# Optimization experiments

Measured on AMD Instinct MI355X. Metric: run time of the kernel, lower is better.

## Reference

```python
import jax, jax.numpy as jnp
import numpy as np

WS = (2, 7, 7)   # window size (d, h, w)
NH = 4           # num heads
EPS = 1e-5       # LayerNorm eps (torch default)


def _rel_index():
    wd, wh, ww = WS
    coords = np.stack(np.meshgrid(np.arange(wd), np.arange(wh), np.arange(ww), indexing='ij'))  # (3,wd,wh,ww)
    cf = coords.reshape(3, -1)                      # (3, N)
    rel = cf[:, :, None] - cf[:, None, :]           # (3, N, N)
    rel = rel.transpose(1, 2, 0).astype(np.int64)   # (N, N, 3)
    rel[..., 0] += wd - 1
    rel[..., 1] += wh - 1
    rel[..., 2] += ww - 1
    rel[..., 0] *= (2 * wh - 1) * (2 * ww - 1)
    rel[..., 1] *= (2 * ww - 1)
    return jnp.asarray(rel.sum(-1), dtype=jnp.int32)  # (N, N)


def setup_inputs() -> dict:
    key = jax.random.key(0)
    ks = jax.random.split(key, 6)
    C, CH = 128, 512
    TBL = (2 * WS[0] - 1) * (2 * WS[1] - 1) * (2 * WS[2] - 1)  # 507
    rn = lambda k, s, sc=0.02: jax.random.normal(k, s, jnp.float32) * sc
    return {
        'x': jax.random.normal(ks[0], (2, 8, 56, 56, C), jnp.float32),
        'norm1_w': jnp.ones((C,), jnp.float32), 'norm1_b': jnp.zeros((C,), jnp.float32),
        'qkv_w': rn(ks[1], (3 * C, C)), 'qkv_b': jnp.zeros((3 * C,), jnp.float32),
        'bias_table': rn(ks[2], (TBL, NH)),
        'proj_w': rn(ks[3], (C, C)), 'proj_b': jnp.zeros((C,), jnp.float32),
        'norm2_w': jnp.ones((C,), jnp.float32), 'norm2_b': jnp.zeros((C,), jnp.float32),
        'fc1_w': rn(ks[4], (CH, C)), 'fc1_b': jnp.zeros((CH,), jnp.float32),
        'fc2_w': rn(ks[5], (C, CH)), 'fc2_b': jnp.zeros((C,), jnp.float32),
        'rel_index': _rel_index(),
    }


def _layernorm(x, w, b):
    m = jnp.mean(x, axis=-1, keepdims=True)
    v = jnp.mean(jnp.square(x - m), axis=-1, keepdims=True)
    return (x - m) * jax.lax.rsqrt(v + EPS) * w + b


def reference(x, norm1_w, norm1_b, qkv_w, qkv_b, bias_table, proj_w, proj_b,
              norm2_w, norm2_b, fc1_w, fc1_b, fc2_w, fc2_b, rel_index):
    B, D, H, W, C = x.shape
    wd, wh, ww = WS
    N = wd * wh * ww
    hd = C // NH

    shortcut = x
    xn = _layernorm(x, norm1_w, norm1_b)
    # window partition: (B,D,H,W,C) -> (B*nW, N, C)
    xw = xn.reshape(B, D // wd, wd, H // wh, wh, W // ww, ww, C)
    xw = xw.transpose(0, 1, 3, 5, 2, 4, 6, 7).reshape(-1, N, C)
    B_ = xw.shape[0]

    qkv = (xw @ qkv_w.T + qkv_b).reshape(B_, N, 3, NH, hd).transpose(2, 0, 3, 1, 4)
    q, k, v = qkv[0] * (hd ** -0.5), qkv[1], qkv[2]   # (B_, NH, N, hd)
    attn = jnp.einsum('bhnd,bhmd->bhnm', q, k)
    bias = bias_table[rel_index.reshape(-1)].reshape(N, N, NH).transpose(2, 0, 1)  # (NH,N,N)
    attn = jax.nn.softmax(attn + bias[None], axis=-1)
    out = jnp.einsum('bhnm,bhmd->bhnd', attn, v).transpose(0, 2, 1, 3).reshape(B_, N, C)
    out = out @ proj_w.T + proj_b

    # window reverse: (B*nW, N, C) -> (B,D,H,W,C)
    xr = out.reshape(B, D // wd, H // wh, W // ww, wd, wh, ww, C)
    xr = xr.transpose(0, 1, 4, 2, 5, 3, 6, 7).reshape(B, D, H, W, C)

    x = shortcut + xr
    h = _layernorm(x, norm2_w, norm2_b)
    h = jax.nn.gelu(h @ fc1_w.T + fc1_b, approximate=False)  # torch nn.GELU = exact erf
    return x + (h @ fc2_w.T + fc2_b)
```

## Files before the change

kernel.cpp:

```cpp
#include <hip/hip_runtime.h>
#include <hip/hip_bf16.h>

typedef __hip_bfloat16 bf16;
typedef unsigned short u16t;
typedef unsigned int u32t;
typedef __attribute__((ext_vector_type(8))) short bf16x8_t;
typedef __attribute__((ext_vector_type(4))) float f32x4_t;

#define DEVI static __device__ __forceinline__

DEVI float u2f(u32t bits) { union { u32t u; float f; } v; v.u = bits; return v.f; }
DEVI float bflo(u32t u) { return u2f((u & 0xffffu) << 16); }
DEVI float bfhi(u32t u) { return u2f(u & 0xffff0000u); }
DEVI float sh2f(short s) { return u2f(((u32t)(u16t)s) << 16); }
DEVI float bf2f(bf16 h) { return __bfloat162float(h); }
DEVI bf16 f2bf(float f) { return __float2bfloat16(f); }
DEVI u16t f2bfbits(float f) {
  bf16 h = __float2bfloat16(f);
  union { bf16 h; u16t u; } v; v.h = h; return v.u;
}

DEVI void gl_lds16(const void* g, void* l) {
  __builtin_amdgcn_global_load_lds(
      (const __attribute__((address_space(1))) unsigned int*)g,
      (__attribute__((address_space(3))) unsigned int*)l, 16, 0, 0);
}

#define TOK   50176
#define NWIN  512
#define NTOK  98
#define NHEAD 4
#define HDIM  32
#define QSCALE 0.17677669529663687f

__global__ __launch_bounds__(256) void setup_k(
    const float* __restrict__ a, const float* __restrict__ b,
    const float* __restrict__ c, const float* __restrict__ d,
    bf16* __restrict__ o,
    const float* __restrict__ btab, const int* __restrict__ relidx,
    const float* __restrict__ qkv_b, float* __restrict__ BmatT,
    float* __restrict__ bsc) {
  int bx = blockIdx.x;
  if (bx < 768) {
    int i = bx * 256 + threadIdx.x;
    const float* s; int off;
    if (i < 49152)       { s = a; off = 0; }
    else if (i < 65536)  { s = b; off = 49152; }
    else if (i < 131072) { s = c; off = 65536; }
    else                 { s = d; off = 131072; }
    float v = s[i - off];
    if (i < 16384) v *= QSCALE;
    o[i] = f2bf(v);
  } else {
    int idx = (bx - 768) * 256 + threadIdx.x;
    if (idx < NTOK * NTOK) {
      int i = idx / NTOK, j = idx - i * NTOK;
      int r = relidx[idx] * NHEAD;
#pragma unroll
      for (int h = 0; h < NHEAD; h++)
        BmatT[(size_t)(h * NTOK + j) * 112 + i] = btab[r + h];
    }
    if (bx == 768 && threadIdx.x < 384)
      bsc[threadIdx.x] = qkv_b[threadIdx.x] * (threadIdx.x < 128 ? QSCALE : 1.0f);
  }
}

DEVI int winrev(int grow) {
  int nw = grow / NTOK, n = grow - nw * NTOK;
  int wq = nw & 7, hq = (nw >> 3) & 7, dq = (nw >> 6) & 3, bb = nw >> 8;
  int wr = n % 7; int q7 = n / 7; int hr = q7 % 7, dr = q7 / 7;
  return ((bb * 8 + dq * 2 + dr) * 56 + hq * 7 + hr) * 56 + wq * 7 + wr;
}

__global__ __launch_bounds__(256) void qkvln_k(
    const float* __restrict__ x, const float* __restrict__ n1w,
    const float* __restrict__ n1b, const bf16* __restrict__ W,
    const float* __restrict__ bsc, bf16* __restrict__ qkvO)
{
  __shared__ __align__(16) short As[64 * 128];
  __shared__ __align__(16) short Bs[128 * 128];
  const int tid = threadIdx.x;
  const int rowBase = blockIdx.x << 6;
  const int wv = tid >> 6, lane = tid & 63;
  const int q = lane >> 4, r16 = lane & 15;

#pragma unroll
  for (int t = 0; t < 8; t++) {
    int f = tid + (t << 8);
    int row = f >> 4, cs = (f & 15) ^ (row & 15);
    gl_lds16((const u16t*)W + (size_t)row * 128 + (cs << 3), &Bs[f << 3]);
  }

  {
    const int c = lane << 1;
    float lw0 = n1w[c], lw1 = n1w[c + 1];
    float lb0 = n1b[c], lb1 = n1b[c + 1];
#pragma unroll
    for (int rr = 0; rr < 16; rr++) {
      int row = (wv << 4) + rr;
      int tt = winrev(rowBase + row);
      float2 xv = *(const float2*)(x + (size_t)tt * 128 + c);
      float x0 = xv.x, x1 = xv.y;
      float s = x0 + x1, ss = x0 * x0 + x1 * x1;
#pragma unroll
      for (int m = 32; m; m >>= 1) { s += __shfl_xor(s, m); ss += __shfl_xor(ss, m); }
      float mean = s * 0.0078125f;
      float var = ss * 0.0078125f - mean * mean;
      float rstd = rsqrtf(var + 1e-5f);
      float y0 = (x0 - mean) * rstd * lw0 + lb0;
      float y1 = (x1 - mean) * rstd * lw1 + lb1;
      u32t ov = ((u32t)f2bfbits(y1) << 16) | (u32t)f2bfbits(y0);
      int slot = (lane >> 2) ^ (row & 15);
      *(u32t*)&As[(row << 7) + (slot << 3) + ((lane & 3) << 1)] = ov;
    }
  }
  __syncthreads();

#pragma unroll 1
  for (int qt = 0; qt < 3; qt++) {
    if (qt > 0) {
#pragma unroll
      for (int t = 0; t < 8; t++) {
        int f = tid + (t << 8);
        int row = f >> 4, cs = (f & 15) ^ (row & 15);
        gl_lds16((const u16t*)W + (size_t)((qt << 7) + row) * 128 + (cs << 3),
                 &Bs[f << 3]);
      }
      __syncthreads();
    }
    f32x4_t acc[8];
#pragma unroll
    for (int j = 0; j < 8; j++) acc[j] = (f32x4_t){0.f, 0.f, 0.f, 0.f};
#pragma unroll
    for (int ks = 0; ks < 4; ks++) {
      int rowA = (wv << 4) + r16;
      int slotA = ((ks << 2) + q) ^ (rowA & 15);
      bf16x8_t af = *(const bf16x8_t*)&As[(rowA << 7) + (slotA << 3)];
      bf16x8_t bfr[8];
#pragma unroll
      for (int nt = 0; nt < 8; nt++) {
        int row = (nt << 4) + r16;
        int slot = ((ks << 2) + q) ^ (row & 15);
        bfr[nt] = *(const bf16x8_t*)&Bs[(row << 7) + (slot << 3)];
      }
#pragma unroll
      for (int nt = 0; nt < 8; nt++)
        acc[nt] = __builtin_amdgcn_mfma_f32_16x16x32_bf16(af, bfr[nt], acc[nt], 0, 0, 0);
    }
    float bv[8];
#pragma unroll
    for (int nt = 0; nt < 8; nt++) bv[nt] = bsc[(qt << 7) + (nt << 4) + r16];
    __syncthreads();
#pragma unroll
    for (int reg = 0; reg < 4; reg++) {
      int lrow = (wv << 4) + (q << 2) + reg;
#pragma unroll
      for (int nt = 0; nt < 8; nt++)
        Bs[(lrow << 7) + (nt << 4) + r16] = (short)f2bfbits(acc[nt][reg] + bv[nt]);
    }
    __syncthreads();
#pragma unroll
    for (int t = 0; t < 4; t++) {
      int f = tid + (t << 8);
      int row = f >> 4, c8 = (f & 15) << 3;
      size_t ob = (size_t)(rowBase + row) * 384 + (qt << 7) + c8;
      *(uint4*)((u16t*)qkvO + ob) = *(const uint4*)&Bs[(row << 7) + c8];
    }
    if (qt < 2) __syncthreads();
  }
}

__global__ __launch_bounds__(512, 4) void proj_k(
    const bf16* __restrict__ A, const bf16* __restrict__ W,
    const float* __restrict__ bias, const float* __restrict__ resX,
    bf16* __restrict__ outB, bf16* __restrict__ outB2,
    const float* __restrict__ lnw, const float* __restrict__ lnb)
{
  __shared__ __align__(16) short As[128 * 128];
  __shared__ __align__(16) short Bs[128 * 128];
  const int tid = threadIdx.x;
  const int rowBase = blockIdx.x << 7;
  const int wv = tid >> 6, lane = tid & 63;
  const int q = lane >> 4, r16 = lane & 15;
  const int mB = wv << 4;

#pragma unroll
  for (int t = 0; t < 4; t++) {
    int f = tid + (t << 9);
    int row = f >> 4, cs = (f & 15) ^ (row & 15);
    gl_lds16((const u16t*)A + (size_t)(rowBase + row) * 128 + (cs << 3),
             &As[f << 3]);
  }
#pragma unroll
  for (int t = 0; t < 4; t++) {
    int f = tid + (t << 9);
    int row = f >> 4, cs = (f & 15) ^ (row & 15);
    gl_lds16((const u16t*)W + (size_t)row * 128 + (cs << 3), &Bs[f << 3]);
  }
  __syncthreads();

  f32x4_t acc[8];
#pragma unroll
  for (int j = 0; j < 8; j++) acc[j] = (f32x4_t){0.f, 0.f, 0.f, 0.f};
#pragma unroll
  for (int ks = 0; ks < 4; ks++) {
    int rowA = mB + r16;
    int slotA = ((ks << 2) + q) ^ (rowA & 15);
    bf16x8_t af = *(const bf16x8_t*)&As[(rowA << 7) + (slotA << 3)];
    bf16x8_t bfr[8];
#pragma unroll
    for (int nt = 0; nt < 8; nt++) {
      int row = (nt << 4) + r16;
      int slot = ((ks << 2) + q) ^ (row & 15);
      bfr[nt] = *(const bf16x8_t*)&Bs[(row << 7) + (slot << 3)];
    }
#pragma unroll
    for (int nt = 0; nt < 8; nt++)
      acc[nt] = __builtin_amdgcn_mfma_f32_16x16x32_bf16(af, bfr[nt], acc[nt], 0, 0, 0);
  }
  __syncthreads();

  float bv[8];
#pragma unroll
  for (int nt = 0; nt < 8; nt++) bv[nt] = bias[(nt << 4) + r16];

#pragma unroll
  for (int reg = 0; reg < 4; reg++) {
    int lrow = mB + (q << 2) + reg;
#pragma unroll
    for (int nt = 0; nt < 8; nt++)
      As[(lrow << 7) + (nt << 4) + r16] = (short)f2bfbits(acc[nt][reg] + bv[nt]);
  }
  __syncthreads();
#pragma unroll
  for (int t = 0; t < 4; t++) {
    int f = tid + (t << 9);
    int row = f >> 4, c8 = (f & 15) << 3;
    int tt = winrev(rowBase + row);
    size_t ob = (size_t)tt * 128 + c8;
    float4 r0 = *(const float4*)(resX + ob);
    float4 r1 = *(const float4*)(resX + ob + 4);
    short* cs = &As[(row << 7) + c8];
    u16t pk[8];
    pk[0] = f2bfbits(sh2f(cs[0]) + r0.x); pk[1] = f2bfbits(sh2f(cs[1]) + r0.y);
    pk[2] = f2bfbits(sh2f(cs[2]) + r0.z); pk[3] = f2bfbits(sh2f(cs[3]) + r0.w);
    pk[4] = f2bfbits(sh2f(cs[4]) + r1.x); pk[5] = f2bfbits(sh2f(cs[5]) + r1.y);
    pk[6] = f2bfbits(sh2f(cs[6]) + r1.z); pk[7] = f2bfbits(sh2f(cs[7]) + r1.w);
    *(uint4*)((u16t*)outB + ob) = *(const uint4*)pk;
    *(uint4*)cs = *(const uint4*)pk;
  }
  __syncthreads();
  const int c = lane << 1;
  float2 lw = *(const float2*)(lnw + c);
  float2 lb = *(const float2*)(lnb + c);
#pragma unroll 4
  for (int rr = 0; rr < 16; rr++) {
    int row = (wv << 4) + rr;
    u32t u = *(const u32t*)&As[(row << 7) + c];
    float x0 = bflo(u), x1 = bfhi(u);
    float s = x0 + x1, ss = x0 * x0 + x1 * x1;
#pragma unroll
    for (int m = 32; m; m >>= 1) { s += __shfl_xor(s, m); ss += __shfl_xor(ss, m); }
    float mean = s * 0.0078125f;
    float var = ss * 0.0078125f - mean * mean;
    float rstd = rsqrtf(var + 1e-5f);
    float y0 = (x0 - mean) * rstd * lw.x + lb.x;
    float y1 = (x1 - mean) * rstd * lw.y + lb.y;
    int tt = winrev(rowBase + row);
    u32t ov = ((u32t)f2bfbits(y1) << 16) | (u32t)f2bfbits(y0);
    *(u32t*)((u16t*)outB2 + (size_t)tt * 128 + c) = ov;
  }
}

__global__ __launch_bounds__(512, 4) void mlp_fused_k(
    const bf16* __restrict__ Axn, const bf16* __restrict__ F1,
    const bf16* __restrict__ F2, const float* __restrict__ b1,
    const float* __restrict__ b2, const bf16* __restrict__ resB,
    float* __restrict__ out)
{
  __shared__ __align__(16) char smem[81920];
  short* As  = (short*)smem;
  short* F1s = (short*)(smem + 32768);
  short* F2s = (short*)(smem + 49152);
  short* Hs  = (short*)(smem + 65536);
  float* Cf  = (float*)smem;

  const int tid = threadIdx.x;
  const int rowBase = blockIdx.x << 7;
  const int wv = tid >> 6, lane = tid & 63;
  const int q = lane >> 4, r16 = lane & 15;
  const int mB = wv << 4;

#pragma unroll
  for (int t = 0; t < 4; t++) {
    int f = tid + (t << 9);
    int row = f >> 4, cs = (f & 15) ^ (row & 15);
    gl_lds16((const u16t*)Axn + (size_t)(rowBase + row) * 128 + (cs << 3),
             &As[f << 3]);
  }
#pragma unroll
  for (int t = 0; t < 2; t++) {
    int f = tid + (t << 9);
    int row = f >> 4, cs = (f & 15) ^ (row & 15);
    gl_lds16((const u16t*)F1 + (size_t)row * 128 + (cs << 3), &F1s[f << 3]);
  }
#pragma unroll
  for (int t = 0; t < 2; t++) {
    int f = tid + (t << 9);
    int row = f >> 3, cs = (f & 7) ^ (row & 7);
    gl_lds16((const u16t*)F2 + (size_t)row * 512 + (cs << 3), &F2s[f << 3]);
  }
  __syncthreads();

  f32x4_t oacc[8];
#pragma unroll
  for (int j = 0; j < 8; j++) oacc[j] = (f32x4_t){0.f, 0.f, 0.f, 0.f};

#pragma unroll 1
  for (int c = 0; c < 8; c++) {
    if (c > 0) {
#pragma unroll
      for (int t = 0; t < 2; t++) {
        int f = tid + (t << 9);
        int row = f >> 4, cs = (f & 15) ^ (row & 15);
        gl_lds16((const u16t*)F1 + (size_t)(c * 64 + row) * 128 + (cs << 3),
                 &F1s[f << 3]);
      }
#pragma unroll
      for (int t = 0; t < 2; t++) {
        int f = tid + (t << 9);
        int row = f >> 3, cs = (f & 7) ^ (row & 7);
        gl_lds16((const u16t*)F2 + (size_t)row * 512 + c * 64 + (cs << 3),
                 &F2s[f << 3]);
      }
      __syncthreads();
    }

    f32x4_t hacc[4];
#pragma unroll
    for (int j = 0; j < 4; j++) hacc[j] = (f32x4_t){0.f, 0.f, 0.f, 0.f};
#pragma unroll
    for (int ks = 0; ks < 4; ks++) {
      int rowA = mB + r16;
      int slotA = ((ks << 2) + q) ^ (rowA & 15);
      bf16x8_t af = *(const bf16x8_t*)&As[(rowA << 7) + (slotA << 3)];
      bf16x8_t bfr[4];
#pragma unroll
      for (int nt = 0; nt < 4; nt++) {
        int row = (nt << 4) + r16;
        int slot = ((ks << 2) + q) ^ (row & 15);
        bfr[nt] = *(const bf16x8_t*)&F1s[(row << 7) + (slot << 3)];
      }
#pragma unroll
      for (int nt = 0; nt < 4; nt++)
        hacc[nt] = __builtin_amdgcn_mfma_f32_16x16x32_bf16(af, bfr[nt], hacc[nt], 0, 0, 0);
    }

    float bb[4];
#pragma unroll
    for (int nt = 0; nt < 4; nt++) bb[nt] = b1[c * 64 + (nt << 4) + r16];
#pragma unroll
    for (int reg = 0; reg < 4; reg++) {
      int lrow = mB + (q << 2) + reg;
#pragma unroll
      for (int nt = 0; nt < 4; nt++) {
        float v = hacc[nt][reg] + bb[nt];
        v = 0.5f * v * (1.0f + erff(v * 0.70710678118654752f));
        int col = (nt << 4) + r16;
        int sp = (col >> 3) ^ (lrow & 7);
        Hs[(lrow << 6) + (sp << 3) + (col & 7)] = (short)f2bfbits(v);
      }
    }
    __syncthreads();

#pragma unroll
    for (int ks = 0; ks < 2; ks++) {
      int rowA = mB + r16;
      int slotA = ((ks << 2) + q) ^ (rowA & 7);
      bf16x8_t af = *(const bf16x8_t*)&Hs[(rowA << 6) + (slotA << 3)];
      bf16x8_t bfr[8];
#pragma unroll
      for (int nt = 0; nt < 8; nt++) {
        int row = (nt << 4) + r16;
        int slot = ((ks << 2) + q) ^ (row & 7);
        bfr[nt] = *(const bf16x8_t*)&F2s[(row << 6) + (slot << 3)];
      }
#pragma unroll
      for (int nt = 0; nt < 8; nt++)
        oacc[nt] = __builtin_amdgcn_mfma_f32_16x16x32_bf16(af, bfr[nt], oacc[nt], 0, 0, 0);
    }
    __syncthreads();
  }

  float bv[8];
#pragma unroll
  for (int nt = 0; nt < 8; nt++) bv[nt] = b2[(nt << 4) + r16];
#pragma unroll
  for (int reg = 0; reg < 4; reg++) {
    int lrow = mB + (q << 2) + reg;
#pragma unroll
    for (int nt = 0; nt < 8; nt++)
      Cf[lrow * 132 + (nt << 4) + r16] = oacc[nt][reg] + bv[nt];
  }
  __syncthreads();
#pragma unroll
  for (int t = 0; t < 8; t++) {
    int f = tid + (t << 9);
    int row = f >> 5, c4 = (f & 31) << 2;
    size_t ob = (size_t)(rowBase + row) * 128 + c4;
    const u16t* rp = (const u16t*)resB + ob;
    const float* cp = &Cf[row * 132 + c4];
    float4 v;
    v.x = cp[0] + sh2f(rp[0]);
    v.y = cp[1] + sh2f(rp[1]);
    v.z = cp[2] + sh2f(rp[2]);
    v.w = cp[3] + sh2f(rp[3]);
    *(float4*)(out + ob) = v;
  }
}

#define PSTR 136
__global__ __launch_bounds__(256) void attn_mfma_k(
    const bf16* __restrict__ qkv, const float* __restrict__ BmatT,
    bf16* __restrict__ out)
{
  __shared__ short Vt[32 * PSTR];
  __shared__ short Ps[112 * PSTR];
  const int nw = blockIdx.x, h = blockIdx.y;
  const int tid = threadIdx.x;
  const int wv = tid >> 6, lane = tid & 63;
  const int q = lane >> 4, r16 = lane & 15;

  for (int idx = tid; idx < 32 * 38; idx += 256) {
    int d = idx / 38, j = 98 + idx % 38;
    Vt[d * PSTR + j] = 0;
  }
  for (int idx = tid; idx < 112 * 12; idx += 256) {
    int r = idx / 12, c = (idx % 12) << 1;
    *(u32t*)&Ps[r * PSTR + 112 + c] = 0;
  }
  for (int idx = tid; idx < NTOK * 16; idx += 256) {
    int j = idx >> 4, d2 = (idx & 15) << 1;
    u32t uv = *(const u32t*)((const u16t*)qkv +
                             (size_t)(nw * NTOK + j) * 384 + 256 + h * 32 + d2);
    Vt[d2 * PSTR + j] = (short)(uv & 0xffffu);
    Vt[(d2 + 1) * PSTR + j] = (short)(uv >> 16);
  }
  __syncthreads();

  const int mt0 = wv;
  const bool has2 = (wv + 4) < 7;
  const int mt1 = has2 ? wv + 4 : wv;

  int i0 = mt0 * 16 + r16; if (i0 > NTOK - 1) i0 = NTOK - 1;
  int i1 = mt1 * 16 + r16; if (i1 > NTOK - 1) i1 = NTOK - 1;
  bf16x8_t aq0 = *(const bf16x8_t*)((const u16t*)qkv +
      (size_t)(nw * NTOK + i0) * 384 + h * 32 + (q << 3));
  bf16x8_t aq1 = *(const bf16x8_t*)((const u16t*)qkv +
      (size_t)(nw * NTOK + i1) * 384 + h * 32 + (q << 3));

  f32x4_t sc[2][7];
#pragma unroll
  for (int nt = 0; nt < 7; nt++) {
    int j = (nt << 4) + r16; if (j > NTOK - 1) j = NTOK - 1;
    const float* bRow = &BmatT[(size_t)(h * NTOK + j) * 112];
    bf16x8_t bk = *(const bf16x8_t*)((const u16t*)qkv +
        (size_t)(nw * NTOK + j) * 384 + 128 + h * 32 + (q << 3));
    f32x4_t b0 = *(const f32x4_t*)&bRow[mt0 * 16 + (q << 2)];
    f32x4_t b1 = *(const f32x4_t*)&bRow[mt1 * 16 + (q << 2)];
    sc[0][nt] = __builtin_amdgcn_mfma_f32_16x16x32_bf16(aq0, bk, b0, 0, 0, 0);
    sc[1][nt] = __builtin_amdgcn_mfma_f32_16x16x32_bf16(aq1, bk, b1, 0, 0, 0);
  }

#pragma unroll
  for (int sel = 0; sel < 2; sel++) {
    if (sel == 1 && !has2) break;
    int mtile = sel ? mt1 : mt0;
    int ibase = mtile * 16 + (q << 2);
    float s[4][7];
#pragma unroll
    for (int nt = 0; nt < 7; nt++) {
      int j = (nt << 4) + r16;
#pragma unroll
      for (int reg = 0; reg < 4; reg++) {
        int i = ibase + reg;
        s[reg][nt] = (i < NTOK && j < NTOK) ? sc[sel][nt][reg] : -1.0e30f;
      }
    }
#pragma unroll
    for (int reg = 0; reg < 4; reg++) {
      float m = -3.0e38f;
#pragma unroll
      for (int nt = 0; nt < 7; nt++) m = fmaxf(m, s[reg][nt]);
#pragma unroll
      for (int d = 8; d; d >>= 1) m = fmaxf(m, __shfl_xor(m, d));
      float sum = 0.f;
#pragma unroll
      for (int nt = 0; nt < 7; nt++) { s[reg][nt] = __expf(s[reg][nt] - m); sum += s[reg][nt]; }
#pragma unroll
      for (int d = 8; d; d >>= 1) sum += __shfl_xor(sum, d);
      float inv = 1.f / sum;
#pragma unroll
      for (int nt = 0; nt < 7; nt++)
        Ps[(ibase + reg) * PSTR + (nt << 4) + r16] =
            (short)f2bfbits(s[reg][nt] * inv);
    }
    f32x4_t o0 = {0.f, 0.f, 0.f, 0.f}, o1 = {0.f, 0.f, 0.f, 0.f};
#pragma unroll
    for (int kt = 0; kt < 4; kt++) {
      bf16x8_t ap = *(const bf16x8_t*)&Ps[(mtile * 16 + r16) * PSTR + (kt << 5) + (q << 3)];
      bf16x8_t bv0 = *(const bf16x8_t*)&Vt[r16 * PSTR + (kt << 5) + (q << 3)];
      bf16x8_t bv1 = *(const bf16x8_t*)&Vt[(16 + r16) * PSTR + (kt << 5) + (q << 3)];
      o0 = __builtin_amdgcn_mfma_f32_16x16x32_bf16(ap, bv0, o0, 0, 0, 0);
      o1 = __builtin_amdgcn_mfma_f32_16x16x32_bf16(ap, bv1, o1, 0, 0, 0);
    }
#pragma unroll
    for (int reg = 0; reg < 4; reg++) {
      int i = mtile * 16 + (q << 2) + reg;
      if (i < NTOK) {
        size_t ob = (size_t)(nw * NTOK + i) * 128 + h * 32;
        out[ob + r16] = f2bf(o0[reg]);
        out[ob + 16 + r16] = f2bf(o1[reg]);
      }
    }
  }
}

extern "C" void kernel_launch(void* const* d_in, const int* in_sizes, int n_in,
                              void* d_out, int out_size, void* d_ws, size_t ws_size,
                              hipStream_t stream) {
  const float* x      = (const float*)d_in[0];
  const float* n1w    = (const float*)d_in[1];
  const float* n1b    = (const float*)d_in[2];
  const float* qkv_w  = (const float*)d_in[3];
  const float* qkv_b  = (const float*)d_in[4];
  const float* btab   = (const float*)d_in[5];
  const float* proj_w = (const float*)d_in[6];
  const float* proj_b = (const float*)d_in[7];
  const float* n2w    = (const float*)d_in[8];
  const float* n2b    = (const float*)d_in[9];
  const float* fc1_w  = (const float*)d_in[10];
  const float* fc1_b  = (const float*)d_in[11];
  const float* fc2_w  = (const float*)d_in[12];
  const float* fc2_b  = (const float*)d_in[13];
  const int*   relidx = (const int*)d_in[14];

  const size_t Asz = (size_t)TOK * 128 * 2;
  char* ws = (char*)d_ws;
  bf16* wbf   = (bf16*)ws;
  bf16* qkvw16  = wbf;
  bf16* projw16 = wbf + 49152;
  bf16* fc1w16  = wbf + 65536;
  bf16* fc2w16  = wbf + 131072;
  float* BmatT = (float*)(ws + 393216);
  float* bsc   = (float*)(ws + 393216 + 175616);
  char* R = ws + (1 << 20);
  bf16* attn  = (bf16*)d_out;
  bf16* qkv   = (bf16*)R;
  bf16* x2    = (bf16*)R;
  bf16* xn2   = (bf16*)(R + Asz);
  float* out  = (float*)d_out;

  setup_k<<<806, 256, 0, stream>>>(qkv_w, proj_w, fc1_w, fc2_w, wbf,
                                   btab, relidx, qkv_b, BmatT, bsc);
  qkvln_k<<<TOK / 64, 256, 0, stream>>>(x, n1w, n1b, qkvw16, bsc, qkv);
  attn_mfma_k<<<dim3(NWIN, NHEAD), 256, 0, stream>>>(qkv, BmatT, attn);
  proj_k<<<TOK / 128, 512, 0, stream>>>(
      attn, projw16, proj_b, x, x2, xn2, n2w, n2b);
  mlp_fused_k<<<TOK / 128, 512, 0, stream>>>(
      xn2, fc1w16, fc2w16, fc1_b, fc2_b, x2, out);
}
```

Before: 207.3 us.

## Fuse projection, residual, LayerNorm2 and MLP into one kernel

Merges the projection kernel and the fused MLP kernel into a single kernel. The projected+residual tile and its LayerNorm result now stay in LDS, and the residual x2 is kept in registers, so the intermediate x2/xn2 bf16 buffers are no longer written to and re-read from global memory, and one launch is removed. The MLP output is now scattered back to window-reversed token positions in the final buffer. The cost is higher register pressure from the 16 held residual words. There is also a possible cross-block hazard: the attention input also lives in the output buffer, so one block's output writes could overwrite attention rows another block has not yet read.

```diff
diff --git a/kernel.cpp b/kernel.cpp
--- a/kernel.cpp
+++ b/kernel.cpp
@@ -170,14 +170,22 @@
   }
 }
 
-__global__ __launch_bounds__(512, 4) void proj_k(
-    const bf16* __restrict__ A, const bf16* __restrict__ W,
-    const float* __restrict__ bias, const float* __restrict__ resX,
-    bf16* __restrict__ outB, bf16* __restrict__ outB2,
-    const float* __restrict__ lnw, const float* __restrict__ lnb)
+__global__ __launch_bounds__(512, 4) void projmlp_k(
+    const bf16* __restrict__ A, const bf16* __restrict__ Wp,
+    const float* __restrict__ pb, const float* __restrict__ resX,
+    const float* __restrict__ lnw, const float* __restrict__ lnb,
+    const bf16* __restrict__ F1, const bf16* __restrict__ F2,
+    const float* __restrict__ b1, const float* __restrict__ b2,
+    float* __restrict__ out)
 {
-  __shared__ __align__(16) short As[128 * 128];
-  __shared__ __align__(16) short Bs[128 * 128];
+  __shared__ __align__(16) char smem[81920];
+  short* As  = (short*)smem;
+  short* Bs  = (short*)(smem + 32768);
+  short* F1s = (short*)(smem + 32768);
+  short* F2s = (short*)(smem + 49152);
+  short* Hs  = (short*)(smem + 65536);
+  float* Cf  = (float*)smem;
+
   const int tid = threadIdx.x;
   const int rowBase = blockIdx.x << 7;
   const int wv = tid >> 6, lane = tid & 63;
@@ -195,7 +203,7 @@
   for (int t = 0; t < 4; t++) {
     int f = tid + (t << 9);
     int row = f >> 4, cs = (f & 15) ^ (row & 15);
-    gl_lds16((const u16t*)W + (size_t)row * 128 + (cs << 3), &Bs[f << 3]);
+    gl_lds16((const u16t*)Wp + (size_t)row * 128 + (cs << 3), &Bs[f << 3]);
   }
   __syncthreads();
 
@@ -220,84 +228,6 @@
   }
   __syncthreads();
 
-  float bv[8];
-#pragma unroll
-  for (int nt = 0; nt < 8; nt++) bv[nt] = bias[(nt << 4) + r16];
-
-#pragma unroll
-  for (int reg = 0; reg < 4; reg++) {
-    int lrow = mB + (q << 2) + reg;
-#pragma unroll
-    for (int nt = 0; nt < 8; nt++)
-      As[(lrow << 7) + (nt << 4) + r16] = (short)f2bfbits(acc[nt][reg] + bv[nt]);
-  }
-  __syncthreads();
-#pragma unroll
-  for (int t = 0; t < 4; t++) {
-    int f = tid + (t << 9);
-    int row = f >> 4, c8 = (f & 15) << 3;
-    int tt = winrev(rowBase + row);
-    size_t ob = (size_t)tt * 128 + c8;
-    float4 r0 = *(const float4*)(resX + ob);
-    float4 r1 = *(const float4*)(resX + ob + 4);
-    short* cs = &As[(row << 7) + c8];
-    u16t pk[8];
-    pk[0] = f2bfbits(sh2f(cs[0]) + r0.x); pk[1] = f2bfbits(sh2f(cs[1]) + r0.y);
-    pk[2] = f2bfbits(sh2f(cs[2]) + r0.z); pk[3] = f2bfbits(sh2f(cs[3]) + r0.w);
-    pk[4] = f2bfbits(sh2f(cs[4]) + r1.x); pk[5] = f2bfbits(sh2f(cs[5]) + r1.y);
-    pk[6] = f2bfbits(sh2f(cs[6]) + r1.z); pk[7] = f2bfbits(sh2f(cs[7]) + r1.w);
-    *(uint4*)((u16t*)outB + ob) = *(const uint4*)pk;
-    *(uint4*)cs = *(const uint4*)pk;
-  }
-  __syncthreads();
-  const int c = lane << 1;
-  float2 lw = *(const float2*)(lnw + c);
-  float2 lb = *(const float2*)(lnb + c);
-#pragma unroll 4
-  for (int rr = 0; rr < 16; rr++) {
-    int row = (wv << 4) + rr;
-    u32t u = *(const u32t*)&As[(row << 7) + c];
-    float x0 = bflo(u), x1 = bfhi(u);
-    float s = x0 + x1, ss = x0 * x0 + x1 * x1;
-#pragma unroll
-    for (int m = 32; m; m >>= 1) { s += __shfl_xor(s, m); ss += __shfl_xor(ss, m); }
-    float mean = s * 0.0078125f;
-    float var = ss * 0.0078125f - mean * mean;
-    float rstd = rsqrtf(var + 1e-5f);
-    float y0 = (x0 - mean) * rstd * lw.x + lb.x;
-    float y1 = (x1 - mean) * rstd * lw.y + lb.y;
-    int tt = winrev(rowBase + row);
-    u32t ov = ((u32t)f2bfbits(y1) << 16) | (u32t)f2bfbits(y0);
-    *(u32t*)((u16t*)outB2 + (size_t)tt * 128 + c) = ov;
-  }
-}
-
-__global__ __launch_bounds__(512, 4) void mlp_fused_k(
-    const bf16* __restrict__ Axn, const bf16* __restrict__ F1,
-    const bf16* __restrict__ F2, const float* __restrict__ b1,
-    const float* __restrict__ b2, const bf16* __restrict__ resB,
-    float* __restrict__ out)
-{
-  __shared__ __align__(16) char smem[81920];
-  short* As  = (short*)smem;
-  short* F1s = (short*)(smem + 32768);
-  short* F2s = (short*)(smem + 49152);
-  short* Hs  = (short*)(smem + 65536);
-  float* Cf  = (float*)smem;
-
-  const int tid = threadIdx.x;
-  const int rowBase = blockIdx.x << 7;
-  const int wv = tid >> 6, lane = tid & 63;
-  const int q = lane >> 4, r16 = lane & 15;
-  const int mB = wv << 4;
-
-#pragma unroll
-  for (int t = 0; t < 4; t++) {
-    int f = tid + (t << 9);
-    int row = f >> 4, cs = (f & 15) ^ (row & 15);
-    gl_lds16((const u16t*)Axn + (size_t)(rowBase + row) * 128 + (cs << 3),
-             &As[f << 3]);
-  }
 #pragma unroll
   for (int t = 0; t < 2; t++) {
     int f = tid + (t << 9);
@@ -309,6 +239,63 @@
     int f = tid + (t << 9);
     int row = f >> 3, cs = (f & 7) ^ (row & 7);
     gl_lds16((const u16t*)F2 + (size_t)row * 512 + (cs << 3), &F2s[f << 3]);
+  }
+
+  float pbv[8];
+#pragma unroll
+  for (int nt = 0; nt < 8; nt++) pbv[nt] = pb[(nt << 4) + r16];
+#pragma unroll
+  for (int reg = 0; reg < 4; reg++) {
+    int lrow = mB + (q << 2) + reg;
+#pragma unroll
+    for (int nt = 0; nt < 8; nt++)
+      As[(lrow << 7) + (nt << 4) + r16] = (short)f2bfbits(acc[nt][reg] + pbv[nt]);
+  }
+  __syncthreads();
+
+  u32t x2r[16];
+#pragma unroll
+  for (int t = 0; t < 8; t++) {
+    int f = tid + (t << 9);
+    int row = f >> 5, c4 = (f & 31) << 2;
+    int tt = winrev(rowBase + row);
+    size_t ob = (size_t)tt * 128 + c4;
+    float4 r0 = *(const float4*)(resX + ob);
+    short* cs = &As[(row << 7) + c4];
+    u16t pk[4];
+    pk[0] = f2bfbits(sh2f(cs[0]) + r0.x);
+    pk[1] = f2bfbits(sh2f(cs[1]) + r0.y);
+    pk[2] = f2bfbits(sh2f(cs[2]) + r0.z);
+    pk[3] = f2bfbits(sh2f(cs[3]) + r0.w);
+    u32t lo = ((u32t)pk[1] << 16) | pk[0];
+    u32t hi = ((u32t)pk[3] << 16) | pk[2];
+    x2r[2 * t] = lo; x2r[2 * t + 1] = hi;
+    uint2 wvv; wvv.x = lo; wvv.y = hi;
+    *(uint2*)cs = wvv;
+  }
+  __syncthreads();
+
+  {
+    const int c = lane << 1;
+    float2 lw = *(const float2*)(lnw + c);
+    float2 lb = *(const float2*)(lnb + c);
+#pragma unroll 4
+    for (int rr = 0; rr < 16; rr++) {
+      int row = (wv << 4) + rr;
+      u32t u = *(const u32t*)&As[(row << 7) + c];
+      float x0 = bflo(u), x1 = bfhi(u);
+      float s = x0 + x1, ss = x0 * x0 + x1 * x1;
+#pragma unroll
+      for (int m = 32; m; m >>= 1) { s += __shfl_xor(s, m); ss += __shfl_xor(ss, m); }
+      float mean = s * 0.0078125f;
+      float var = ss * 0.0078125f - mean * mean;
+      float rstd = rsqrtf(var + 1e-5f);
+      float y0 = (x0 - mean) * rstd * lw.x + lb.x;
+      float y1 = (x1 - mean) * rstd * lw.y + lb.y;
+      u32t ov = ((u32t)f2bfbits(y1) << 16) | (u32t)f2bfbits(y0);
+      int slot = (lane >> 2) ^ (row & 15);
+      *(u32t*)&As[(row << 7) + (slot << 3) + ((lane & 3) << 1)] = ov;
+    }
   }
   __syncthreads();
 
@@ -407,14 +394,15 @@
   for (int t = 0; t < 8; t++) {
     int f = tid + (t << 9);
     int row = f >> 5, c4 = (f & 31) << 2;
-    size_t ob = (size_t)(rowBase + row) * 128 + c4;
-    const u16t* rp = (const u16t*)resB + ob;
+    int tt = winrev(rowBase + row);
+    size_t ob = (size_t)tt * 128 + c4;
     const float* cp = &Cf[row * 132 + c4];
+    u32t lo = x2r[2 * t], hi = x2r[2 * t + 1];
     float4 v;
-    v.x = cp[0] + sh2f(rp[0]);
-    v.y = cp[1] + sh2f(rp[1]);
-    v.z = cp[2] + sh2f(rp[2]);
-    v.w = cp[3] + sh2f(rp[3]);
+    v.x = cp[0] + bflo(lo);
+    v.y = cp[1] + bfhi(lo);
+    v.z = cp[2] + bflo(hi);
+    v.w = cp[3] + bfhi(hi);
     *(float4*)(out + ob) = v;
   }
 }
@@ -546,6 +534,7 @@
   const int*   relidx = (const int*)d_in[14];
 
   const size_t Asz = (size_t)TOK * 128 * 2;
+  (void)Asz;
   char* ws = (char*)d_ws;
   bf16* wbf   = (bf16*)ws;
   bf16* qkvw16  = wbf;
@@ -557,16 +546,13 @@
   char* R = ws + (1 << 20);
   bf16* attn  = (bf16*)d_out;
   bf16* qkv   = (bf16*)R;
-  bf16* x2    = (bf16*)R;
-  bf16* xn2   = (bf16*)(R + Asz);
   float* out  = (float*)d_out;
 
   setup_k<<<806, 256, 0, stream>>>(qkv_w, proj_w, fc1_w, fc2_w, wbf,
                                    btab, relidx, qkv_b, BmatT, bsc);
   qkvln_k<<<TOK / 64, 256, 0, stream>>>(x, n1w, n1b, qkvw16, bsc, qkv);
   attn_mfma_k<<<dim3(NWIN, NHEAD), 256, 0, stream>>>(qkv, BmatT, attn);
-  proj_k<<<TOK / 128, 512, 0, stream>>>(
-      attn, projw16, proj_b, x, x2, xn2, n2w, n2b);
-  mlp_fused_k<<<TOK / 128, 512, 0, stream>>>(
-      xn2, fc1w16, fc2w16, fc1_b, fc2_b, x2, out);
-}
+  projmlp_k<<<TOK / 128, 512, 0, stream>>>(
+      attn, projw16, proj_b, x, n2w, n2b,
+      fc1w16, fc2w16, fc1_b, fc2_b, out);
+}
```

Measured after the change: 209.7 us. About the same (+1.2%).
